# Performance work log

Measured on AMD Instinct MI355X. Metric: run time of the kernel, lower is better.

Reference implementation:

```python
import jax, jax.numpy as jnp
import numpy as np

NUM_CLASSES = 13
MIN_PTS = 50
CLUSTER_THRESHOLD = 0.3
MAX_CLUSTERS = 10
PROB_THRESH = 0.05


def _fps_indices(pts, valid, S):
    # Deterministic farthest-point sampling restricted to `valid` points.
    # Invalid points get min-distance -inf so they are never selected.
    neg = jnp.where(valid, 0.0, -jnp.inf)  # [N]
    start = jnp.argmax(valid)  # first valid point

    def d2_to(i):
        return jnp.sum((pts - pts[i]) ** 2, axis=-1)  # [N]

    mind = d2_to(start) + neg

    def step(mind, _):
        nxt = jnp.argmax(mind)
        mind = jnp.minimum(mind, d2_to(nxt) + neg)
        return mind, nxt

    _, rest = jax.lax.scan(step, mind, None, length=S - 1)
    return jnp.concatenate([start[None], rest])  # [S]


def _per_class(shifted, prob):
    # shifted: [N,3] shifted coords; prob: [N] softmax prob of this class.
    valid = prob > PROB_THRESH
    count = jnp.sum(valid)
    # num_seeds = min(max_clusters, count // min_pts, count); seeds k >= num_seeds are masked out
    num_seeds = jnp.minimum(jnp.minimum(MAX_CLUSTERS, count // MIN_PTS), count)
    idx = _fps_indices(shifted, valid, MAX_CLUSTERS)
    seeds = shifted[idx]  # [S,3]
    d2 = jnp.sum((shifted[:, None, :] - seeds[None, :, :]) ** 2, axis=-1)  # [N,S]
    sigma = CLUSTER_THRESHOLD * 0.5
    w = jnp.exp(-d2 / (2.0 * sigma * sigma))  # Gaussian soft ball query
    seed_valid = jnp.arange(MAX_CLUSTERS) < num_seeds  # [S]
    w = w * seed_valid[None, :].astype(w.dtype)
    assign = w / (jnp.sum(w, axis=-1, keepdims=True) + 1e-8)  # soft assignment over seeds
    # scatter into full mask == multiply by class prob gated by threshold membership
    final = assign * (prob * valid.astype(prob.dtype))[:, None]  # [N,S]
    return final.T, seed_valid  # [S,N], [S]


def _forward(semantic_logits, points, offsets):
    probs = jax.nn.softmax(semantic_logits, axis=-1)  # [B,N,C]
    shifted = points + offsets  # [B,N,3]
    per_class_all = jax.vmap(_per_class, in_axes=(None, 1))  # map over classes

    def per_batch(sh, pr):
        masks, seed_valid = per_class_all(sh, pr)  # [C,S,N], [C,S]
        K = NUM_CLASSES * MAX_CLUSTERS
        masks = masks.reshape(K, -1)  # [K,N]
        sv = seed_valid.reshape(K)
        # softmax(mask*10) over instance axis, restricted to valid instance rows
        logits = jnp.where(sv[:, None], masks * 10.0, -jnp.inf)
        out = jax.nn.softmax(logits, axis=0)
        return jnp.where(sv[:, None], out, 0.0)

    return jax.vmap(per_batch)(shifted, probs)  # [B, C*S, N]


def setup_inputs() -> dict:
    key = jax.random.key(0)
    k1, k2, k3 = jax.random.split(key, 3)
    B, N, C = 2, 65536, NUM_CLASSES
    semantic_logits = jax.random.normal(k1, (B, N, C), dtype=jnp.float32)
    points = jax.random.uniform(k2, (B, N, 3), dtype=jnp.float32)  # unit cube
    offsets = jax.random.normal(k3, (B, N, 3), dtype=jnp.float32) * 0.05  # small predicted shifts
    return {"semantic_logits": semantic_logits, "points": points, "offsets": offsets}


def reference(semantic_logits, points, offsets):
    return _forward(semantic_logits, points, offsets)
```

## Files before the change

### kernel.cpp

```cpp
#include <hip/hip_runtime.h>
#include <cstdint>

#define NCLS 13
#define SMAX 10
#define PTHRESH 0.05f
#define FPS_SEG 8
#define FPS_T 512
#define FPS_PPT 16
#define NSLOT 8
#define BCPAD 32
#define GABLK 256
#define BB 2
#define SLOT_DWORDS (BB * NCLS * SMAX * NSLOT * 2)

__device__ __forceinline__ float d2f(float ax, float ay, float az,
                                     float bx, float by, float bz) {
    float dx = ax - bx;
    float dy = ay - by;
    float dz = az - bz;
    return __fadd_rn(__fadd_rn(__fmul_rn(dx, dx), __fmul_rn(dy, dy)), __fmul_rn(dz, dz));
}

__device__ __forceinline__ unsigned int fmono(float f) {
    unsigned int u = __float_as_uint(f);
    return (u & 0x80000000u) ? ~u : (u | 0x80000000u);
}

__global__ void k_setup(const float* __restrict__ logits, const float* __restrict__ pts,
                        const float* __restrict__ offs, float* __restrict__ probs,
                        float* __restrict__ sx, float* __restrict__ sy, float* __restrict__ sz,
                        unsigned int* __restrict__ pcnt, unsigned int* __restrict__ pfst,
                        unsigned int* __restrict__ slots32, int N) {
    int b = blockIdx.y;
    int n = blockIdx.x * blockDim.x + threadIdx.x;
    int t = threadIdx.x;
    __shared__ unsigned int sC[NCLS], sF[NCLS];
    if (t < NCLS) { sC[t] = 0u; sF[t] = 0xFFFFFFFFu; }
    __syncthreads();

    if (b == 0) {
        for (unsigned int i = blockIdx.x * blockDim.x + t; i < SLOT_DWORDS;
             i += GABLK * 256)
            slots32[i] = 0u;
    }

    if (n < N) {
        size_t bn = (size_t)b * N + n;
        const float* L = logits + bn * NCLS;
        float v[NCLS];
        float mx = -INFINITY;
#pragma unroll
        for (int c = 0; c < NCLS; ++c) { v[c] = L[c]; mx = fmaxf(mx, v[c]); }
        float s = 0.f;
#pragma unroll
        for (int c = 0; c < NCLS; ++c) { v[c] = expf(v[c] - mx); s += v[c]; }
        int lane = t & 63;
        int wave_base = n - lane;
#pragma unroll
        for (int c = 0; c < NCLS; ++c) {
            float p = v[c] / s;
            probs[((size_t)b * NCLS + c) * N + n] = p;
            unsigned long long m = __ballot(p > PTHRESH);
            if (lane == 0 && m) {
                atomicAdd(&sC[c], (unsigned int)__popcll(m));
                atomicMin(&sF[c], (unsigned int)(wave_base + __ffsll(m) - 1));
            }
        }
        float x = pts[bn * 3 + 0] + offs[bn * 3 + 0];
        float y = pts[bn * 3 + 1] + offs[bn * 3 + 1];
        float z = pts[bn * 3 + 2] + offs[bn * 3 + 2];
        sx[bn] = x; sy[bn] = y; sz[bn] = z;
    }
    __syncthreads();
    if (t < NCLS) {
        pcnt[(b * NCLS + t) * GABLK + blockIdx.x] = sC[t];
        pfst[(b * NCLS + t) * GABLK + blockIdx.x] = sF[t];
    }
}

__global__ __launch_bounds__(FPS_T, 1) void k_fps(
    const float* __restrict__ probs,
    const float* __restrict__ sx, const float* __restrict__ sy, const float* __restrict__ sz,
    const unsigned int* __restrict__ pcnt, const unsigned int* __restrict__ pfst,
    int* __restrict__ nseeds, float* __restrict__ seedxyz,
    unsigned long long* __restrict__ slots, int N) {
    int bid = blockIdx.x;
    int bc = bid & (BCPAD - 1);
    int g = bid >> 5;
    if (bc >= BB * NCLS) return;
    int b = bc / NCLS;
    int t = threadIdx.x, lane = t & 63, w = t >> 6;

    const unsigned int* pc = pcnt + (size_t)bc * GABLK;
    const unsigned int* pf = pfst + (size_t)bc * GABLK;
    uint4 c4 = *(const uint4*)(pc + lane * 4);
    uint4 f4 = *(const uint4*)(pf + lane * 4);
    unsigned int cnt = c4.x + c4.y + c4.z + c4.w;
    unsigned int fst = min(min(f4.x, f4.y), min(f4.z, f4.w));
#pragma unroll
    for (int off = 1; off < 64; off <<= 1) {
        cnt += __shfl_xor(cnt, off, 64);
        fst = min(fst, __shfl_xor(fst, off, 64));
    }
    int ns = min(SMAX, min((int)cnt / 50, (int)cnt));
    if (g == 0 && t == 0) nseeds[bc] = ns;
    if (ns == 0) return;

    const float* px = sx + (size_t)b * N;
    const float* py = sy + (size_t)b * N;
    const float* pz = sz + (size_t)b * N;
    const float* pp = probs + (size_t)bc * N;

    int base = g * (FPS_T * FPS_PPT) + t;
    float X[FPS_PPT], Y[FPS_PPT], Z[FPS_PPT], m[FPS_PPT];
    unsigned int vm = 0;
#pragma unroll
    for (int j = 0; j < FPS_PPT; ++j) {
        int n = base + (j << 9);
        X[j] = px[n]; Y[j] = py[n]; Z[j] = pz[n];
        if (pp[n] > PTHRESH) vm |= (1u << j);
        m[j] = INFINITY;
    }

    int st = (int)fst;
    float cx = px[st], cy = py[st], cz = pz[st];
    if (g == 0 && t == 0) {
        float* sd = seedxyz + (size_t)bc * SMAX * 3;
        sd[0] = cx; sd[1] = cy; sd[2] = cz;
    }

    __shared__ unsigned long long s_keys[FPS_T / 64];
    __shared__ unsigned long long s_win;

    for (int s = 1; s < ns; ++s) {
        float best = -INFINITY;
        int bidx = 0;
#pragma unroll
        for (int j = 0; j < FPS_PPT; ++j) {
            int n = base + (j << 9);
            float d2 = d2f(X[j], Y[j], Z[j], cx, cy, cz);
            float add = ((vm >> j) & 1u) ? 0.0f : -INFINITY;
            float nm = fminf(m[j], __fadd_rn(d2, add));
            m[j] = nm;
            if (nm > best) { best = nm; bidx = n; }
        }
        unsigned long long key =
            ((unsigned long long)fmono(best) << 32) | (unsigned int)(~(unsigned int)bidx);
#pragma unroll
        for (int off = 1; off < 64; off <<= 1) {
            unsigned long long ok = __shfl_xor(key, off, 64);
            if (ok > key) key = ok;
        }
        if (lane == 0) s_keys[w] = key;
        __syncthreads();

        if (w == 0) {
            unsigned long long bk = (lane < 8) ? s_keys[lane] : 0ULL;
#pragma unroll
            for (int off = 1; off < 8; off <<= 1) {
                unsigned long long ok = __shfl_xor(bk, off, 8);
                if (ok > bk) bk = ok;
            }
            unsigned long long* sl = slots + ((size_t)bc * SMAX + s) * NSLOT;
            if (lane == 0)
                __hip_atomic_store(&sl[g], bk, __ATOMIC_RELAXED, __HIP_MEMORY_SCOPE_AGENT);
            asm volatile("" ::: "memory");
            unsigned long long kk = 0ULL;
            while (true) {
                if (lane < NSLOT && kk == 0ULL)
                    kk = __hip_atomic_load(&sl[lane], __ATOMIC_RELAXED,
                                           __HIP_MEMORY_SCOPE_AGENT);
                if (__all(kk != 0ULL || lane >= NSLOT)) break;
                __builtin_amdgcn_s_sleep(1);
            }
            asm volatile("" ::: "memory");
#pragma unroll
            for (int off = 1; off < 8; off <<= 1) {
                unsigned long long ok = __shfl_xor(kk, off, 8);
                if (ok > kk) kk = ok;
            }
            if (lane == 0) s_win = kk;
        }
        __syncthreads();

        int widx = (int)(~(unsigned int)s_win);
        cx = px[widx]; cy = py[widx]; cz = pz[widx];
        if (g == 0 && t == 0) {
            float* sd = seedxyz + ((size_t)bc * SMAX + s) * 3;
            sd[0] = cx; sd[1] = cy; sd[2] = cz;
        }
        __syncthreads();
    }
}

__global__ __launch_bounds__(512) void k_out(
    const float* __restrict__ probs,
    const float* __restrict__ sx, const float* __restrict__ sy,
    const float* __restrict__ sz,
    const int* __restrict__ nseeds, const float* __restrict__ seedxyz,
    float* __restrict__ out, int N) {
    int b = blockIdx.y;
    int t = threadIdx.x;
    int lane = t & 63;
    int wv = t >> 6;
    int n = blockIdx.x * 64 + lane;

    __shared__ float S[NCLS * SMAX * 3];
    __shared__ int NSs[NCLS];
    __shared__ float gdS[NCLS][64];
    __shared__ float psum[8][64];
    if (t < NCLS * SMAX * 3) S[t] = seedxyz[(size_t)b * NCLS * SMAX * 3 + t];
    if (t >= 448 && t < 448 + NCLS) NSs[t - 448] = nseeds[b * NCLS + (t - 448)];
    __syncthreads();

    size_t bn = (size_t)b * N + n;
    float x = sx[bn], y = sy[bn], z = sz[bn];

    const float kinv = 22.2222222f;
    float ps = 0.f;
#pragma unroll
    for (int c = wv; c < NCLS; c += 8) {
        int ns = NSs[c];
        float gdv = 0.f;
        if (ns > 0) {
            float pv = probs[((size_t)b * NCLS + c) * N + n];
            if (pv > PTHRESH) {
                float wbuf[SMAX];
                float sw = 0.f;
#pragma unroll
                for (int s = 0; s < SMAX; ++s) {
                    wbuf[s] = 0.f;
                    if (s < ns) {
                        const float* sd = &S[(c * SMAX + s) * 3];
                        float d2 = d2f(x, y, z, sd[0], sd[1], sd[2]);
                        wbuf[s] = __expf(-d2 * kinv);
                        sw += wbuf[s];
                    }
                }
                gdv = __fdividef(pv, sw + 1e-8f);
#pragma unroll
                for (int s = 0; s < SMAX; ++s)
                    if (s < ns) ps += __expf(10.f * wbuf[s] * gdv);
            } else {
                ps += (float)ns;
            }
        }
        gdS[c][lane] = gdv;
    }
    psum[wv][lane] = ps;
    __syncthreads();

    float tot = 0.f;
#pragma unroll
    for (int w = 0; w < 8; ++w) tot += psum[w][lane];
    float inv = __fdividef(1.f, tot);

    float* ob = out + (size_t)b * (NCLS * SMAX) * N + n;
#pragma unroll
    for (int k = 0; k < NCLS * SMAX; k += 8) {
        int kk = k + wv;
        if (kk >= NCLS * SMAX) break;
        int c = kk / SMAX, s = kk - c * SMAX;
        float o = 0.f;
        if (s < NSs[c]) {
            float gdv = gdS[c][lane];
            if (gdv > 0.f) {
                const float* sd = &S[(c * SMAX + s) * 3];
                float d2 = d2f(x, y, z, sd[0], sd[1], sd[2]);
                float wval = __expf(-d2 * kinv);
                o = __expf(10.f * wval * gdv) * inv;
            } else {
                o = inv;
            }
        }
        ob[(size_t)kk * N] = o;
    }
}

extern "C" void kernel_launch(void* const* d_in, const int* in_sizes, int n_in,
                              void* d_out, int out_size, void* d_ws, size_t ws_size,
                              hipStream_t stream) {
    const float* logits = (const float*)d_in[0];
    const float* pts    = (const float*)d_in[1];
    const float* offs   = (const float*)d_in[2];
    float* out = (float*)d_out;

    const int B = BB;
    const int BN = in_sizes[0] / NCLS;
    const int N = BN / B;

    char* w = (char*)d_ws;
    size_t off = 0;
    auto take = [&](size_t bytes) -> void* {
        void* p = w + off;
        off = (off + bytes + 255) & ~(size_t)255;
        return p;
    };
    float* probs   = (float*)take((size_t)B * NCLS * N * sizeof(float));
    float* sx      = (float*)take((size_t)B * N * sizeof(float));
    float* sy      = (float*)take((size_t)B * N * sizeof(float));
    float* sz      = (float*)take((size_t)B * N * sizeof(float));
    float* seedxyz = (float*)take((size_t)B * NCLS * SMAX * 3 * sizeof(float));
    unsigned int* pcnt = (unsigned int*)take((size_t)B * NCLS * GABLK * sizeof(unsigned int));
    unsigned int* pfst = (unsigned int*)take((size_t)B * NCLS * GABLK * sizeof(unsigned int));
    int* nseeds        = (int*)take(B * NCLS * sizeof(int));
    unsigned long long* slots =
        (unsigned long long*)take((size_t)B * NCLS * SMAX * NSLOT * sizeof(unsigned long long));

    dim3 gA((N + 255) / 256, B);
    k_setup<<<gA, 256, 0, stream>>>(logits, pts, offs, probs, sx, sy, sz,
                                    pcnt, pfst, (unsigned int*)slots, N);

    k_fps<<<BCPAD * FPS_SEG, FPS_T, 0, stream>>>(probs, sx, sy, sz, pcnt, pfst,
                                                 nseeds, seedxyz, slots, N);

    dim3 gC(N / 64, B);
    k_out<<<gC, 512, 0, stream>>>(probs, sx, sy, sz, nseeds, seedxyz, out, N);
}
```

Measured before the change: 65.73 us.

## Pack shifted points as float4 with class bitmask; all waves poll FPS slots; 2 points per thread in output

Setup now writes shifted coordinates as a packed float4 array and a 16-bit per-point validity mask over classes. FPS reads these instead of three SoA arrays plus the per-class probability array, which cuts the load traffic of its prologue. In the FPS loop every wave now polls the cross-block slots itself, with double-buffered shared keys and no sleep, which removes two block barriers per step at the cost of more polling traffic. The output kernel handles two points per thread with float2 loads and stores over half as many blocks.

```diff
diff --git a/kernel.cpp b/kernel.cpp
--- a/kernel.cpp
+++ b/kernel.cpp
@@ -28,7 +28,7 @@
 
 __global__ void k_setup(const float* __restrict__ logits, const float* __restrict__ pts,
                         const float* __restrict__ offs, float* __restrict__ probs,
-                        float* __restrict__ sx, float* __restrict__ sy, float* __restrict__ sz,
+                        float4* __restrict__ xyzw, unsigned short* __restrict__ vmask,
                         unsigned int* __restrict__ pcnt, unsigned int* __restrict__ pfst,
                         unsigned int* __restrict__ slots32, int N) {
     int b = blockIdx.y;
@@ -56,11 +56,14 @@
         for (int c = 0; c < NCLS; ++c) { v[c] = expf(v[c] - mx); s += v[c]; }
         int lane = t & 63;
         int wave_base = n - lane;
+        unsigned int msk = 0;
 #pragma unroll
         for (int c = 0; c < NCLS; ++c) {
             float p = v[c] / s;
             probs[((size_t)b * NCLS + c) * N + n] = p;
-            unsigned long long m = __ballot(p > PTHRESH);
+            bool valid = p > PTHRESH;
+            if (valid) msk |= (1u << c);
+            unsigned long long m = __ballot(valid);
             if (lane == 0 && m) {
                 atomicAdd(&sC[c], (unsigned int)__popcll(m));
                 atomicMin(&sF[c], (unsigned int)(wave_base + __ffsll(m) - 1));
@@ -69,7 +72,8 @@
         float x = pts[bn * 3 + 0] + offs[bn * 3 + 0];
         float y = pts[bn * 3 + 1] + offs[bn * 3 + 1];
         float z = pts[bn * 3 + 2] + offs[bn * 3 + 2];
-        sx[bn] = x; sy[bn] = y; sz[bn] = z;
+        xyzw[bn] = make_float4(x, y, z, 0.f);
+        vmask[bn] = (unsigned short)msk;
     }
     __syncthreads();
     if (t < NCLS) {
@@ -79,8 +83,7 @@
 }
 
 __global__ __launch_bounds__(FPS_T, 1) void k_fps(
-    const float* __restrict__ probs,
-    const float* __restrict__ sx, const float* __restrict__ sy, const float* __restrict__ sz,
+    const float4* __restrict__ xyzw, const unsigned short* __restrict__ vmask,
     const unsigned int* __restrict__ pcnt, const unsigned int* __restrict__ pfst,
     int* __restrict__ nseeds, float* __restrict__ seedxyz,
     unsigned long long* __restrict__ slots, int N) {
@@ -89,6 +92,7 @@
     int g = bid >> 5;
     if (bc >= BB * NCLS) return;
     int b = bc / NCLS;
+    int c = bc - b * NCLS;
     int t = threadIdx.x, lane = t & 63, w = t >> 6;
 
     const unsigned int* pc = pcnt + (size_t)bc * GABLK;
@@ -106,10 +110,8 @@
     if (g == 0 && t == 0) nseeds[bc] = ns;
     if (ns == 0) return;
 
-    const float* px = sx + (size_t)b * N;
-    const float* py = sy + (size_t)b * N;
-    const float* pz = sz + (size_t)b * N;
-    const float* pp = probs + (size_t)bc * N;
+    const float4* P4 = xyzw + (size_t)b * N;
+    const unsigned short* VM = vmask + (size_t)b * N;
 
     int base = g * (FPS_T * FPS_PPT) + t;
     float X[FPS_PPT], Y[FPS_PPT], Z[FPS_PPT], m[FPS_PPT];
@@ -117,20 +119,21 @@
 #pragma unroll
     for (int j = 0; j < FPS_PPT; ++j) {
         int n = base + (j << 9);
-        X[j] = px[n]; Y[j] = py[n]; Z[j] = pz[n];
-        if (pp[n] > PTHRESH) vm |= (1u << j);
+        float4 q = P4[n];
+        X[j] = q.x; Y[j] = q.y; Z[j] = q.z;
+        if ((VM[n] >> c) & 1) vm |= (1u << j);
         m[j] = INFINITY;
     }
 
     int st = (int)fst;
-    float cx = px[st], cy = py[st], cz = pz[st];
+    float4 q0 = P4[st];
+    float cx = q0.x, cy = q0.y, cz = q0.z;
     if (g == 0 && t == 0) {
         float* sd = seedxyz + (size_t)bc * SMAX * 3;
         sd[0] = cx; sd[1] = cy; sd[2] = cz;
     }
 
-    __shared__ unsigned long long s_keys[FPS_T / 64];
-    __shared__ unsigned long long s_win;
+    __shared__ unsigned long long s_keys[2][FPS_T / 64];
 
     for (int s = 1; s < ns; ++s) {
         float best = -INFINITY;
@@ -151,129 +154,157 @@
             unsigned long long ok = __shfl_xor(key, off, 64);
             if (ok > key) key = ok;
         }
-        if (lane == 0) s_keys[w] = key;
+        int par = s & 1;
+        if (lane == 0) s_keys[par][w] = key;
         __syncthreads();
 
+        unsigned long long* sl = slots + ((size_t)bc * SMAX + s) * NSLOT;
         if (w == 0) {
-            unsigned long long bk = (lane < 8) ? s_keys[lane] : 0ULL;
+            unsigned long long bk = (lane < 8) ? s_keys[par][lane] : 0ULL;
 #pragma unroll
             for (int off = 1; off < 8; off <<= 1) {
                 unsigned long long ok = __shfl_xor(bk, off, 8);
                 if (ok > bk) bk = ok;
             }
-            unsigned long long* sl = slots + ((size_t)bc * SMAX + s) * NSLOT;
             if (lane == 0)
                 __hip_atomic_store(&sl[g], bk, __ATOMIC_RELAXED, __HIP_MEMORY_SCOPE_AGENT);
-            asm volatile("" ::: "memory");
-            unsigned long long kk = 0ULL;
-            while (true) {
-                if (lane < NSLOT && kk == 0ULL)
-                    kk = __hip_atomic_load(&sl[lane], __ATOMIC_RELAXED,
-                                           __HIP_MEMORY_SCOPE_AGENT);
-                if (__all(kk != 0ULL || lane >= NSLOT)) break;
-                __builtin_amdgcn_s_sleep(1);
-            }
-            asm volatile("" ::: "memory");
-#pragma unroll
-            for (int off = 1; off < 8; off <<= 1) {
-                unsigned long long ok = __shfl_xor(kk, off, 8);
-                if (ok > kk) kk = ok;
-            }
-            if (lane == 0) s_win = kk;
-        }
-        __syncthreads();
-
-        int widx = (int)(~(unsigned int)s_win);
-        cx = px[widx]; cy = py[widx]; cz = pz[widx];
+        }
+        asm volatile("" ::: "memory");
+        unsigned long long kk = 0ULL;
+        while (true) {
+            if (lane < NSLOT && kk == 0ULL)
+                kk = __hip_atomic_load(&sl[lane], __ATOMIC_RELAXED,
+                                       __HIP_MEMORY_SCOPE_AGENT);
+            if (__all(kk != 0ULL || lane >= NSLOT)) break;
+        }
+        asm volatile("" ::: "memory");
+#pragma unroll
+        for (int off = 1; off < 8; off <<= 1) {
+            unsigned long long ok = __shfl_xor(kk, off, 8);
+            if (ok > kk) kk = ok;
+        }
+        kk = __shfl(kk, 0, 64);
+
+        int widx = (int)(~(unsigned int)kk);
+        float4 qw = P4[widx];
+        cx = qw.x; cy = qw.y; cz = qw.z;
         if (g == 0 && t == 0) {
             float* sd = seedxyz + ((size_t)bc * SMAX + s) * 3;
             sd[0] = cx; sd[1] = cy; sd[2] = cz;
         }
-        __syncthreads();
     }
 }
 
 __global__ __launch_bounds__(512) void k_out(
-    const float* __restrict__ probs,
-    const float* __restrict__ sx, const float* __restrict__ sy,
-    const float* __restrict__ sz,
+    const float* __restrict__ probs, const float4* __restrict__ xyzw,
     const int* __restrict__ nseeds, const float* __restrict__ seedxyz,
     float* __restrict__ out, int N) {
     int b = blockIdx.y;
     int t = threadIdx.x;
     int lane = t & 63;
     int wv = t >> 6;
-    int n = blockIdx.x * 64 + lane;
+    int n0 = blockIdx.x * 128 + lane * 2;
 
     __shared__ float S[NCLS * SMAX * 3];
     __shared__ int NSs[NCLS];
-    __shared__ float gdS[NCLS][64];
-    __shared__ float psum[8][64];
+    __shared__ float gdS[NCLS][128];
+    __shared__ float psum[8][128];
     if (t < NCLS * SMAX * 3) S[t] = seedxyz[(size_t)b * NCLS * SMAX * 3 + t];
     if (t >= 448 && t < 448 + NCLS) NSs[t - 448] = nseeds[b * NCLS + (t - 448)];
     __syncthreads();
 
-    size_t bn = (size_t)b * N + n;
-    float x = sx[bn], y = sy[bn], z = sz[bn];
+    float4 q0 = xyzw[(size_t)b * N + n0];
+    float4 q1 = xyzw[(size_t)b * N + n0 + 1];
 
     const float kinv = 22.2222222f;
-    float ps = 0.f;
+    float ps0 = 0.f, ps1 = 0.f;
 #pragma unroll
     for (int c = wv; c < NCLS; c += 8) {
         int ns = NSs[c];
-        float gdv = 0.f;
+        float gdv0 = 0.f, gdv1 = 0.f;
         if (ns > 0) {
-            float pv = probs[((size_t)b * NCLS + c) * N + n];
-            if (pv > PTHRESH) {
-                float wbuf[SMAX];
-                float sw = 0.f;
+            float2 pv = *(const float2*)(probs + ((size_t)b * NCLS + c) * N + n0);
+            if (pv.x > PTHRESH) {
+                float wb[SMAX]; float sw = 0.f;
 #pragma unroll
                 for (int s = 0; s < SMAX; ++s) {
-                    wbuf[s] = 0.f;
+                    wb[s] = 0.f;
                     if (s < ns) {
                         const float* sd = &S[(c * SMAX + s) * 3];
-                        float d2 = d2f(x, y, z, sd[0], sd[1], sd[2]);
-                        wbuf[s] = __expf(-d2 * kinv);
-                        sw += wbuf[s];
+                        float d2 = d2f(q0.x, q0.y, q0.z, sd[0], sd[1], sd[2]);
+                        wb[s] = __expf(-d2 * kinv);
+                        sw += wb[s];
                     }
                 }
-                gdv = __fdividef(pv, sw + 1e-8f);
+                gdv0 = __fdividef(pv.x, sw + 1e-8f);
 #pragma unroll
                 for (int s = 0; s < SMAX; ++s)
-                    if (s < ns) ps += __expf(10.f * wbuf[s] * gdv);
+                    if (s < ns) ps0 += __expf(10.f * wb[s] * gdv0);
             } else {
-                ps += (float)ns;
-            }
-        }
-        gdS[c][lane] = gdv;
-    }
-    psum[wv][lane] = ps;
+                ps0 += (float)ns;
+            }
+            if (pv.y > PTHRESH) {
+                float wb[SMAX]; float sw = 0.f;
+#pragma unroll
+                for (int s = 0; s < SMAX; ++s) {
+                    wb[s] = 0.f;
+                    if (s < ns) {
+                        const float* sd = &S[(c * SMAX + s) * 3];
+                        float d2 = d2f(q1.x, q1.y, q1.z, sd[0], sd[1], sd[2]);
+                        wb[s] = __expf(-d2 * kinv);
+                        sw += wb[s];
+                    }
+                }
+                gdv1 = __fdividef(pv.y, sw + 1e-8f);
+#pragma unroll
+                for (int s = 0; s < SMAX; ++s)
+                    if (s < ns) ps1 += __expf(10.f * wb[s] * gdv1);
+            } else {
+                ps1 += (float)ns;
+            }
+        }
+        gdS[c][lane * 2] = gdv0;
+        gdS[c][lane * 2 + 1] = gdv1;
+    }
+    psum[wv][lane * 2] = ps0;
+    psum[wv][lane * 2 + 1] = ps1;
     __syncthreads();
 
-    float tot = 0.f;
-#pragma unroll
-    for (int w = 0; w < 8; ++w) tot += psum[w][lane];
-    float inv = __fdividef(1.f, tot);
-
-    float* ob = out + (size_t)b * (NCLS * SMAX) * N + n;
+    float tot0 = 0.f, tot1 = 0.f;
+#pragma unroll
+    for (int w = 0; w < 8; ++w) {
+        tot0 += psum[w][lane * 2];
+        tot1 += psum[w][lane * 2 + 1];
+    }
+    float inv0 = __fdividef(1.f, tot0);
+    float inv1 = __fdividef(1.f, tot1);
+
+    float* ob = out + (size_t)b * (NCLS * SMAX) * N + n0;
 #pragma unroll
     for (int k = 0; k < NCLS * SMAX; k += 8) {
         int kk = k + wv;
         if (kk >= NCLS * SMAX) break;
         int c = kk / SMAX, s = kk - c * SMAX;
-        float o = 0.f;
+        float o0 = 0.f, o1 = 0.f;
         if (s < NSs[c]) {
-            float gdv = gdS[c][lane];
-            if (gdv > 0.f) {
-                const float* sd = &S[(c * SMAX + s) * 3];
-                float d2 = d2f(x, y, z, sd[0], sd[1], sd[2]);
-                float wval = __expf(-d2 * kinv);
-                o = __expf(10.f * wval * gdv) * inv;
+            float g0 = gdS[c][lane * 2];
+            float g1 = gdS[c][lane * 2 + 1];
+            const float* sd = &S[(c * SMAX + s) * 3];
+            if (g0 > 0.f) {
+                float d2 = d2f(q0.x, q0.y, q0.z, sd[0], sd[1], sd[2]);
+                o0 = __expf(10.f * __expf(-d2 * kinv) * g0) * inv0;
             } else {
-                o = inv;
-            }
-        }
-        ob[(size_t)kk * N] = o;
+                o0 = inv0;
+            }
+            if (g1 > 0.f) {
+                float d2 = d2f(q1.x, q1.y, q1.z, sd[0], sd[1], sd[2]);
+                o1 = __expf(10.f * __expf(-d2 * kinv) * g1) * inv1;
+            } else {
+                o1 = inv1;
+            }
+        }
+        float2 st; st.x = o0; st.y = o1;
+        *(float2*)(ob + (size_t)kk * N) = st;
     }
 }
 
@@ -297,9 +328,8 @@
         return p;
     };
     float* probs   = (float*)take((size_t)B * NCLS * N * sizeof(float));
-    float* sx      = (float*)take((size_t)B * N * sizeof(float));
-    float* sy      = (float*)take((size_t)B * N * sizeof(float));
-    float* sz      = (float*)take((size_t)B * N * sizeof(float));
+    float4* xyzw   = (float4*)take((size_t)B * N * sizeof(float4));
+    unsigned short* vmsk = (unsigned short*)take((size_t)B * N * sizeof(unsigned short));
     float* seedxyz = (float*)take((size_t)B * NCLS * SMAX * 3 * sizeof(float));
     unsigned int* pcnt = (unsigned int*)take((size_t)B * NCLS * GABLK * sizeof(unsigned int));
     unsigned int* pfst = (unsigned int*)take((size_t)B * NCLS * GABLK * sizeof(unsigned int));
@@ -308,12 +338,12 @@
         (unsigned long long*)take((size_t)B * NCLS * SMAX * NSLOT * sizeof(unsigned long long));
 
     dim3 gA((N + 255) / 256, B);
-    k_setup<<<gA, 256, 0, stream>>>(logits, pts, offs, probs, sx, sy, sz,
+    k_setup<<<gA, 256, 0, stream>>>(logits, pts, offs, probs, xyzw, vmsk,
                                     pcnt, pfst, (unsigned int*)slots, N);
 
-    k_fps<<<BCPAD * FPS_SEG, FPS_T, 0, stream>>>(probs, sx, sy, sz, pcnt, pfst,
+    k_fps<<<BCPAD * FPS_SEG, FPS_T, 0, stream>>>(xyzw, vmsk, pcnt, pfst,
                                                  nseeds, seedxyz, slots, N);
 
-    dim3 gC(N / 64, B);
-    k_out<<<gC, 512, 0, stream>>>(probs, sx, sy, sz, nseeds, seedxyz, out, N);
-}
+    dim3 gC(N / 128, B);
+    k_out<<<gC, 512, 0, stream>>>(probs, xyzw, nseeds, seedxyz, out, N);
+}
```

New measurement: 64.16 us. 2.4% less time.
